# Kernel optimization log

Measured on AMD Instinct MI355X. Metric: run time of the kernel, lower is better.

The kernel has to match this reference:

```python
import jax, jax.numpy as jnp
import numpy as np


def setup_inputs() -> dict:
    key = jax.random.key(0)
    ks = jax.random.split(key, 8)
    H = 256  # hidden_size
    NH = 8   # num_heads
    HD = H // NH
    B, G = 256, 1024
    s = 1.0 / np.sqrt(H)
    return {
        "query": jax.random.normal(ks[0], (B, 2 * H), dtype=jnp.float32),
        "ref": jax.random.normal(ks[1], (B, G, H), dtype=jnp.float32),
        "Wq": jax.random.normal(ks[2], (H, 2 * H), dtype=jnp.float32) * s,
        "bq": jax.random.normal(ks[3], (H,), dtype=jnp.float32) * s,
        "We": jax.random.normal(ks[4], (H, H), dtype=jnp.float32) * s,
        "be": jax.random.normal(ks[5], (H,), dtype=jnp.float32) * s,
        "Wv": jax.random.normal(ks[6], (HD,), dtype=jnp.float32) * (1.0 / np.sqrt(HD)),
        "bv": jax.random.normal(ks[7], (1,), dtype=jnp.float32) * 0.01,
        "num_heads": 8,
    }


def reference(query, ref, Wq, bq, We, be, Wv, bv, num_heads):
    B, G, H = ref.shape
    hd = H // num_heads
    # q_dense: [B, 2H] -> [B, H] -> [B, nh, hd]
    q = (query @ Wq.T + bq).reshape(B, num_heads, hd)
    # e_dense: [B, G, H] -> [B, G, H] -> [B, G, nh, hd]
    e = (jnp.einsum('bgh,oh->bgo', ref, We) + be).reshape(B, G, num_heads, hd)
    # broadcast-add over graph dim, tanh, per-head linear scorer (hd -> 1)
    v = jnp.tanh(q[:, None, :, :] + e)                 # [B, G, nh, hd]
    s = jnp.einsum('bgnd,d->bgn', v, Wv) + bv[0]       # [B, G, nh]
    # sum over heads, output [B, 1, G] (matches sum(dim=1).transpose(1,2))
    return s.sum(axis=-1)[:, None, :]
```

## Files before the change

kernel.cpp:

```cpp
#include <hip/hip_runtime.h>

typedef __attribute__((ext_vector_type(8))) short short8;
typedef __attribute__((ext_vector_type(8))) unsigned short ushort8;
typedef __attribute__((ext_vector_type(4))) float f32x4;
typedef unsigned short ushort;
typedef unsigned int uint;

__device__ __forceinline__ float fast_exp2(float x) {
#if __has_builtin(__builtin_amdgcn_exp2f)
    return __builtin_amdgcn_exp2f(x);
#else
    return __expf(x * 0.6931471805599453f);
#endif
}
__device__ __forceinline__ float fast_rcp(float x) {
#if __has_builtin(__builtin_amdgcn_rcpf)
    return __builtin_amdgcn_rcpf(x);
#else
    return __frcp_rn(x);
#endif
}

__device__ __forceinline__ ushort f2bf(float f) {
    uint x = __float_as_uint(f);
    x += 0x7fffu + ((x >> 16) & 1u);
    return (ushort)(x >> 16);
}

__device__ __forceinline__ uint pack2bf(float x, float y) {
    uint xi = __float_as_uint(x) + 0x8000u;
    uint yi = __float_as_uint(y) + 0x8000u;
    return __builtin_amdgcn_perm(yi, xi, 0x07060302u);
}

__global__ __launch_bounds__(256) void prep(
    const float* __restrict__ query, const float* __restrict__ Wq,
    const float* __restrict__ bq, const float* __restrict__ be,
    const float* __restrict__ We, const float* __restrict__ Wv,
    const float* __restrict__ bv, float* __restrict__ q_ws,
    ushort* __restrict__ Web, float* __restrict__ aux) {
    __shared__ float qrow[512];
    const int t = threadIdx.x;
    if (blockIdx.x < 64) {
        const int i = (blockIdx.x * 256 + t) * 4;
        float4 v = *(const float4*)(We + i);
        ushort4 u;
        u.x = f2bf(v.x); u.y = f2bf(v.y); u.z = f2bf(v.z); u.w = f2bf(v.w);
        *(ushort4*)(Web + i) = u;
        return;
    }
    if (blockIdx.x == 320) {
        if (t >= 64) return;
        float v = (t < 32) ? Wv[t] : 0.f;
#pragma unroll
        for (int off = 1; off < 32; off <<= 1) v += __shfl_xor(v, off, 64);
        if (t == 0) aux[0] = 8.f * (v + bv[0]);
        return;
    }
    const int b = blockIdx.x - 64;
    qrow[t]       = query[b * 512 + t];
    qrow[t + 256] = query[b * 512 + 256 + t];
    __syncthreads();
    const f32x4* wr = (const f32x4*)(Wq + (size_t)t * 512);
    float s0 = 0.f, s1 = 0.f, s2 = 0.f, s3 = 0.f;
#pragma unroll 8
    for (int j = 0; j < 128; j += 4) {
        f32x4 w0 = wr[j], w1 = wr[j + 1], w2 = wr[j + 2], w3 = wr[j + 3];
        f32x4 q0 = *(const f32x4*)(qrow + 4 * j);
        f32x4 q1 = *(const f32x4*)(qrow + 4 * j + 4);
        f32x4 q2 = *(const f32x4*)(qrow + 4 * j + 8);
        f32x4 q3 = *(const f32x4*)(qrow + 4 * j + 12);
        s0 += w0.x * q0.x + w0.y * q0.y + w0.z * q0.z + w0.w * q0.w;
        s1 += w1.x * q1.x + w1.y * q1.y + w1.z * q1.z + w1.w * q1.w;
        s2 += w2.x * q2.x + w2.y * q2.y + w2.z * q2.z + w2.w * q2.w;
        s3 += w3.x * q3.x + w3.y * q3.y + w3.z * q3.z + w3.w * q3.w;
    }
    q_ws[b * 256 + t] = (s0 + s1) + (s2 + s3) + bq[t] + be[t];
}

#define BM 64

__global__ __launch_bounds__(256, 3) void fused_gemm(
    const float* __restrict__ ref, const ushort* __restrict__ Web,
    const float* __restrict__ q_ws, const float* __restrict__ Wv,
    const float* __restrict__ aux, float* __restrict__ out) {
    __shared__ uint4 Asm[2048];
    __shared__ float red[4][64];

    const int t = threadIdx.x;
    const int w = t >> 6;
    const int l = t & 63;
    const int quad = l >> 4;
    const int lr = l & 15;
    const size_t row0 = (size_t)blockIdx.x * BM;
    const int b = (int)(row0 >> 10);

    {
        const float* ap = ref + (row0 + w * 16 + lr) * 256 + quad * 8;
#pragma unroll
        for (int half = 0; half < 2; ++half) {
            float4 f[8];
#pragma unroll
            for (int kb = 0; kb < 4; ++kb) {
                f[2 * kb]     = *(const float4*)(ap + (half * 4 + kb) * 32);
                f[2 * kb + 1] = *(const float4*)(ap + (half * 4 + kb) * 32 + 4);
            }
#pragma unroll
            for (int kb = 0; kb < 4; ++kb) {
                uint4 p;
                p.x = pack2bf(f[2 * kb].x,     f[2 * kb].y);
                p.y = pack2bf(f[2 * kb].z,     f[2 * kb].w);
                p.z = pack2bf(f[2 * kb + 1].x, f[2 * kb + 1].y);
                p.w = pack2bf(f[2 * kb + 1].z, f[2 * kb + 1].w);
                Asm[(w * 8 + half * 4 + kb) * 64 + l] = p;
            }
        }
    }

    const ushort* Bp = Web + ((size_t)(w * 64 + lr)) * 256 + quad * 8;
    short8 bcur[4];
#pragma unroll
    for (int cb = 0; cb < 4; ++cb)
        bcur[cb] = *(const short8*)(Bp + cb * 16 * 256);

    const float c2l = 2.885390081777927f;
    const float* qe = q_ws + b * 256;
    const float w2a = -2.f * Wv[lr];
    const float w2b = -2.f * Wv[16 + lr];
    float qvc[4];
#pragma unroll
    for (int cb = 0; cb < 4; ++cb) qvc[cb] = qe[w * 64 + cb * 16 + lr] * c2l;

    __syncthreads();

    f32x4 acc[4][4];
#pragma unroll
    for (int i = 0; i < 4; ++i)
#pragma unroll
        for (int j = 0; j < 4; ++j) acc[i][j] = (f32x4){0.f, 0.f, 0.f, 0.f};

    const ushort* As = (const ushort*)Asm;
#pragma unroll
    for (int k = 0; k < 8; ++k) {
        short8 bnxt[4];
        if (k < 7) {
#pragma unroll
            for (int cb = 0; cb < 4; ++cb)
                bnxt[cb] = *(const short8*)(Bp + cb * 16 * 256 + (k + 1) * 32);
        }
        short8 afr[4];
#pragma unroll
        for (int rb = 0; rb < 4; ++rb)
            afr[rb] = *(const short8*)(As + ((rb * 8 + k) * 64 + l) * 8);
#pragma unroll
        for (int rb = 0; rb < 4; ++rb)
#pragma unroll
            for (int cb = 0; cb < 4; ++cb)
                acc[rb][cb] = __builtin_amdgcn_mfma_f32_16x16x32_bf16(
                    afr[rb], bcur[cb], acc[rb][cb], 0, 0, 0);
        if (k < 7) {
#pragma unroll
            for (int cb = 0; cb < 4; ++cb) bcur[cb] = bnxt[cb];
        }
    }

    float part[4][4];
#pragma unroll
    for (int rb = 0; rb < 4; ++rb)
#pragma unroll
        for (int r = 0; r < 4; ++r) part[rb][r] = 0.f;

#pragma unroll
    for (int cb = 0; cb < 4; ++cb) {
        const float w2 = (cb & 1) ? w2b : w2a;
#pragma unroll
        for (int rb = 0; rb < 4; ++rb)
#pragma unroll
            for (int r = 0; r < 4; ++r) {
                float e = fast_exp2(fmaf(acc[rb][cb][r], c2l, qvc[cb]));
                part[rb][r] = fmaf(w2, fast_rcp(e + 1.f), part[rb][r]);
            }
    }
#pragma unroll
    for (int off = 1; off < 16; off <<= 1)
#pragma unroll
        for (int rb = 0; rb < 4; ++rb)
#pragma unroll
            for (int r = 0; r < 4; ++r)
                part[rb][r] += __shfl_xor(part[rb][r], off, 64);

    if (lr == 0) {
#pragma unroll
        for (int rb = 0; rb < 4; ++rb)
#pragma unroll
            for (int r = 0; r < 4; ++r)
                red[w][rb * 16 + quad * 4 + r] = part[rb][r];
    }
    __syncthreads();
    if (t < 64) {
        float s = red[0][t] + red[1][t] + red[2][t] + red[3][t] + aux[0];
        out[row0 + t] = s;
    }
}

extern "C" void kernel_launch(void* const* d_in, const int* in_sizes, int n_in,
                              void* d_out, int out_size, void* d_ws, size_t ws_size,
                              hipStream_t stream) {
    const float* query = (const float*)d_in[0];
    const float* ref   = (const float*)d_in[1];
    const float* Wq    = (const float*)d_in[2];
    const float* bq    = (const float*)d_in[3];
    const float* We    = (const float*)d_in[4];
    const float* be    = (const float*)d_in[5];
    const float* Wv    = (const float*)d_in[6];
    const float* bv    = (const float*)d_in[7];
    float* out = (float*)d_out;

    float*  q_ws = (float*)d_ws;
    ushort* Web  = (ushort*)((char*)d_ws + 262144);
    float*  aux  = (float*)((char*)d_ws + 262144 + 131072);

    prep<<<321, 256, 0, stream>>>(query, Wq, bq, be, We, Wv, bv, q_ws, Web, aux);
    fused_gemm<<<4096, 256, 0, stream>>>(ref, Web, q_ws, Wv, aux, out);
}
```

Before: 423.0 us.

## Load A fragments directly into registers with 2x2 wave tiling, drop LDS staging

The GEMM kernel no longer stages the bf16-converted ref tile in shared memory. Waves are now arranged 2x2, each owning 32 rows by 128 columns, and each loads its A fragments straight from global memory into registers, converting to bf16 in place. This removes the LDS write/read round trip and the barrier before the MFMA loop, and halves redundant A loads per wave. In exchange, B loads per wave double, register pressure rises, and launch bounds occupancy drops from 3 to 2 blocks per CU.

```diff
diff --git a/kernel.cpp b/kernel.cpp
--- a/kernel.cpp
+++ b/kernel.cpp
@@ -1,7 +1,6 @@
 #include <hip/hip_runtime.h>
 
 typedef __attribute__((ext_vector_type(8))) short short8;
-typedef __attribute__((ext_vector_type(8))) unsigned short ushort8;
 typedef __attribute__((ext_vector_type(4))) float f32x4;
 typedef unsigned short ushort;
 typedef unsigned int uint;
@@ -31,6 +30,15 @@
     uint xi = __float_as_uint(x) + 0x8000u;
     uint yi = __float_as_uint(y) + 0x8000u;
     return __builtin_amdgcn_perm(yi, xi, 0x07060302u);
+}
+
+__device__ __forceinline__ short8 pack8(float4 a, float4 b) {
+    union { uint4 u; short8 s; } c;
+    c.u.x = pack2bf(a.x, a.y);
+    c.u.y = pack2bf(a.z, a.w);
+    c.u.z = pack2bf(b.x, b.y);
+    c.u.w = pack2bf(b.z, b.w);
+    return c.s;
 }
 
 __global__ __launch_bounds__(256) void prep(
@@ -80,126 +88,120 @@
 
 #define BM 64
 
-__global__ __launch_bounds__(256, 3) void fused_gemm(
+__global__ __launch_bounds__(256, 2) void fused_gemm(
     const float* __restrict__ ref, const ushort* __restrict__ Web,
     const float* __restrict__ q_ws, const float* __restrict__ Wv,
     const float* __restrict__ aux, float* __restrict__ out) {
-    __shared__ uint4 Asm[2048];
-    __shared__ float red[4][64];
+    __shared__ float red[2][64];
 
     const int t = threadIdx.x;
     const int w = t >> 6;
+    const int wr = w >> 1;
+    const int wc = w & 1;
     const int l = t & 63;
     const int quad = l >> 4;
     const int lr = l & 15;
     const size_t row0 = (size_t)blockIdx.x * BM;
     const int b = (int)(row0 >> 10);
 
-    {
-        const float* ap = ref + (row0 + w * 16 + lr) * 256 + quad * 8;
-#pragma unroll
-        for (int half = 0; half < 2; ++half) {
-            float4 f[8];
-#pragma unroll
-            for (int kb = 0; kb < 4; ++kb) {
-                f[2 * kb]     = *(const float4*)(ap + (half * 4 + kb) * 32);
-                f[2 * kb + 1] = *(const float4*)(ap + (half * 4 + kb) * 32 + 4);
-            }
-#pragma unroll
-            for (int kb = 0; kb < 4; ++kb) {
-                uint4 p;
-                p.x = pack2bf(f[2 * kb].x,     f[2 * kb].y);
-                p.y = pack2bf(f[2 * kb].z,     f[2 * kb].w);
-                p.z = pack2bf(f[2 * kb + 1].x, f[2 * kb + 1].y);
-                p.w = pack2bf(f[2 * kb + 1].z, f[2 * kb + 1].w);
-                Asm[(w * 8 + half * 4 + kb) * 64 + l] = p;
-            }
+    const float* ap = ref + (row0 + wr * 32 + lr) * 256 + quad * 8;
+    const ushort* Bp = Web + ((size_t)(wc * 128 + lr)) * 256 + quad * 8;
+
+    short8 bc[8];
+#pragma unroll
+    for (int cb = 0; cb < 8; ++cb)
+        bc[cb] = *(const short8*)(Bp + cb * 16 * 256);
+
+    short8 af[2][8];
+#pragma unroll
+    for (int k = 0; k < 4; ++k) {
+        float4 a0 = *(const float4*)(ap + k * 32);
+        float4 a1 = *(const float4*)(ap + k * 32 + 4);
+        float4 a2 = *(const float4*)(ap + 16 * 256 + k * 32);
+        float4 a3 = *(const float4*)(ap + 16 * 256 + k * 32 + 4);
+        af[0][k] = pack8(a0, a1);
+        af[1][k] = pack8(a2, a3);
+    }
+    __builtin_amdgcn_sched_barrier(0);
+#pragma unroll
+    for (int k = 4; k < 8; ++k) {
+        float4 a0 = *(const float4*)(ap + k * 32);
+        float4 a1 = *(const float4*)(ap + k * 32 + 4);
+        float4 a2 = *(const float4*)(ap + 16 * 256 + k * 32);
+        float4 a3 = *(const float4*)(ap + 16 * 256 + k * 32 + 4);
+        af[0][k] = pack8(a0, a1);
+        af[1][k] = pack8(a2, a3);
+    }
+
+    f32x4 acc[2][8];
+#pragma unroll
+    for (int i = 0; i < 2; ++i)
+#pragma unroll
+        for (int j = 0; j < 8; ++j) acc[i][j] = (f32x4){0.f, 0.f, 0.f, 0.f};
+
+#pragma unroll
+    for (int k = 0; k < 8; ++k) {
+        short8 bn[8];
+        if (k < 7) {
+#pragma unroll
+            for (int cb = 0; cb < 8; ++cb)
+                bn[cb] = *(const short8*)(Bp + cb * 16 * 256 + (k + 1) * 32);
         }
-    }
-
-    const ushort* Bp = Web + ((size_t)(w * 64 + lr)) * 256 + quad * 8;
-    short8 bcur[4];
-#pragma unroll
-    for (int cb = 0; cb < 4; ++cb)
-        bcur[cb] = *(const short8*)(Bp + cb * 16 * 256);
+#pragma unroll
+        for (int rt = 0; rt < 2; ++rt)
+#pragma unroll
+            for (int cb = 0; cb < 8; ++cb)
+                acc[rt][cb] = __builtin_amdgcn_mfma_f32_16x16x32_bf16(
+                    af[rt][k], bc[cb], acc[rt][cb], 0, 0, 0);
+        if (k < 7) {
+#pragma unroll
+            for (int cb = 0; cb < 8; ++cb) bc[cb] = bn[cb];
+        }
+    }
 
     const float c2l = 2.885390081777927f;
-    const float* qe = q_ws + b * 256;
+    const float* qe = q_ws + b * 256 + wc * 128 + lr;
     const float w2a = -2.f * Wv[lr];
     const float w2b = -2.f * Wv[16 + lr];
-    float qvc[4];
-#pragma unroll
-    for (int cb = 0; cb < 4; ++cb) qvc[cb] = qe[w * 64 + cb * 16 + lr] * c2l;
-
-    __syncthreads();
-
-    f32x4 acc[4][4];
-#pragma unroll
-    for (int i = 0; i < 4; ++i)
-#pragma unroll
-        for (int j = 0; j < 4; ++j) acc[i][j] = (f32x4){0.f, 0.f, 0.f, 0.f};
-
-    const ushort* As = (const ushort*)Asm;
-#pragma unroll
-    for (int k = 0; k < 8; ++k) {
-        short8 bnxt[4];
-        if (k < 7) {
-#pragma unroll
-            for (int cb = 0; cb < 4; ++cb)
-                bnxt[cb] = *(const short8*)(Bp + cb * 16 * 256 + (k + 1) * 32);
-        }
-        short8 afr[4];
-#pragma unroll
-        for (int rb = 0; rb < 4; ++rb)
-            afr[rb] = *(const short8*)(As + ((rb * 8 + k) * 64 + l) * 8);
-#pragma unroll
-        for (int rb = 0; rb < 4; ++rb)
-#pragma unroll
-            for (int cb = 0; cb < 4; ++cb)
-                acc[rb][cb] = __builtin_amdgcn_mfma_f32_16x16x32_bf16(
-                    afr[rb], bcur[cb], acc[rb][cb], 0, 0, 0);
-        if (k < 7) {
-#pragma unroll
-            for (int cb = 0; cb < 4; ++cb) bcur[cb] = bnxt[cb];
-        }
-    }
-
-    float part[4][4];
-#pragma unroll
-    for (int rb = 0; rb < 4; ++rb)
-#pragma unroll
-        for (int r = 0; r < 4; ++r) part[rb][r] = 0.f;
-
-#pragma unroll
-    for (int cb = 0; cb < 4; ++cb) {
+    float qv[8];
+#pragma unroll
+    for (int cb = 0; cb < 8; ++cb) qv[cb] = qe[cb * 16] * c2l;
+
+    float part[2][4];
+#pragma unroll
+    for (int rt = 0; rt < 2; ++rt)
+#pragma unroll
+        for (int r = 0; r < 4; ++r) part[rt][r] = 0.f;
+
+#pragma unroll
+    for (int cb = 0; cb < 8; ++cb) {
         const float w2 = (cb & 1) ? w2b : w2a;
 #pragma unroll
-        for (int rb = 0; rb < 4; ++rb)
+        for (int rt = 0; rt < 2; ++rt)
 #pragma unroll
             for (int r = 0; r < 4; ++r) {
-                float e = fast_exp2(fmaf(acc[rb][cb][r], c2l, qvc[cb]));
-                part[rb][r] = fmaf(w2, fast_rcp(e + 1.f), part[rb][r]);
+                float e = fast_exp2(fmaf(acc[rt][cb][r], c2l, qv[cb]));
+                part[rt][r] = fmaf(w2, fast_rcp(e + 1.f), part[rt][r]);
             }
     }
 #pragma unroll
     for (int off = 1; off < 16; off <<= 1)
 #pragma unroll
-        for (int rb = 0; rb < 4; ++rb)
+        for (int rt = 0; rt < 2; ++rt)
 #pragma unroll
             for (int r = 0; r < 4; ++r)
-                part[rb][r] += __shfl_xor(part[rb][r], off, 64);
+                part[rt][r] += __shfl_xor(part[rt][r], off, 64);
 
     if (lr == 0) {
 #pragma unroll
-        for (int rb = 0; rb < 4; ++rb)
+        for (int rt = 0; rt < 2; ++rt)
 #pragma unroll
             for (int r = 0; r < 4; ++r)
-                red[w][rb * 16 + quad * 4 + r] = part[rb][r];
+                red[wc][wr * 32 + rt * 16 + quad * 4 + r] = part[rt][r];
     }
     __syncthreads();
     if (t < 64) {
-        float s = red[0][t] + red[1][t] + red[2][t] + red[3][t] + aux[0];
-        out[row0 + t] = s;
+        out[row0 + t] = red[0][t] + red[1][t] + aux[0];
     }
 }
 
```

After: 496.3 us. 1.17x slower.

## Make fused GEMM persistent over row tiles with resident B and double-buffered A

Applied to the files above, without the earlier changes.

Each block now processes 512 rows in 16 tiles of 32 rows and keeps the entire bf16 We slice it needs in registers, so it loads it once per block instead of once per 64 rows. The ref loads for the next tile are issued before the MFMAs on the current tile and written into a second LDS buffer, overlapping global loads with compute. Output reduction writes are deferred by one iteration. The trade-offs are a much larger register footprint (occupancy bound lowered to 2), only 512 blocks, and a barrier per tile.

```diff
diff --git a/kernel.cpp b/kernel.cpp
--- a/kernel.cpp
+++ b/kernel.cpp
@@ -1,7 +1,6 @@
 #include <hip/hip_runtime.h>
 
 typedef __attribute__((ext_vector_type(8))) short short8;
-typedef __attribute__((ext_vector_type(8))) unsigned short ushort8;
 typedef __attribute__((ext_vector_type(4))) float f32x4;
 typedef unsigned short ushort;
 typedef unsigned int uint;
@@ -31,6 +30,15 @@
     uint xi = __float_as_uint(x) + 0x8000u;
     uint yi = __float_as_uint(y) + 0x8000u;
     return __builtin_amdgcn_perm(yi, xi, 0x07060302u);
+}
+
+__device__ __forceinline__ uint4 pack8u(float4 a, float4 b) {
+    uint4 c;
+    c.x = pack2bf(a.x, a.y);
+    c.y = pack2bf(a.z, a.w);
+    c.z = pack2bf(b.x, b.y);
+    c.w = pack2bf(b.z, b.w);
+    return c;
 }
 
 __global__ __launch_bounds__(256) void prep(
@@ -78,128 +86,145 @@
     q_ws[b * 256 + t] = (s0 + s1) + (s2 + s3) + bq[t] + be[t];
 }
 
-#define BM 64
-
-__global__ __launch_bounds__(256, 3) void fused_gemm(
+__global__ __launch_bounds__(256, 2) void fused_gemm(
     const float* __restrict__ ref, const ushort* __restrict__ Web,
     const float* __restrict__ q_ws, const float* __restrict__ Wv,
     const float* __restrict__ aux, float* __restrict__ out) {
-    __shared__ uint4 Asm[2048];
-    __shared__ float red[4][64];
+    __shared__ uint4 Asm[2 * 1024];
+    __shared__ float red[2][4][32];
 
     const int t = threadIdx.x;
     const int w = t >> 6;
     const int l = t & 63;
     const int quad = l >> 4;
     const int lr = l & 15;
-    const size_t row0 = (size_t)blockIdx.x * BM;
-    const int b = (int)(row0 >> 10);
-
-    {
-        const float* ap = ref + (row0 + w * 16 + lr) * 256 + quad * 8;
-#pragma unroll
-        for (int half = 0; half < 2; ++half) {
-            float4 f[8];
-#pragma unroll
-            for (int kb = 0; kb < 4; ++kb) {
-                f[2 * kb]     = *(const float4*)(ap + (half * 4 + kb) * 32);
-                f[2 * kb + 1] = *(const float4*)(ap + (half * 4 + kb) * 32 + 4);
-            }
-#pragma unroll
-            for (int kb = 0; kb < 4; ++kb) {
-                uint4 p;
-                p.x = pack2bf(f[2 * kb].x,     f[2 * kb].y);
-                p.y = pack2bf(f[2 * kb].z,     f[2 * kb].w);
-                p.z = pack2bf(f[2 * kb + 1].x, f[2 * kb + 1].y);
-                p.w = pack2bf(f[2 * kb + 1].z, f[2 * kb + 1].w);
-                Asm[(w * 8 + half * 4 + kb) * 64 + l] = p;
-            }
-        }
-    }
+    const int rbw = w & 1;
+    const int kh = w >> 1;
+    const size_t rowB = (size_t)blockIdx.x * 512;
+    const int b = (int)(blockIdx.x >> 1);
 
     const ushort* Bp = Web + ((size_t)(w * 64 + lr)) * 256 + quad * 8;
-    short8 bcur[4];
+    short8 bfr[4][8];
 #pragma unroll
     for (int cb = 0; cb < 4; ++cb)
-        bcur[cb] = *(const short8*)(Bp + cb * 16 * 256);
+#pragma unroll
+        for (int k = 0; k < 8; ++k)
+            bfr[cb][k] = *(const short8*)(Bp + cb * 16 * 256 + k * 32);
 
     const float c2l = 2.885390081777927f;
     const float* qe = q_ws + b * 256;
     const float w2a = -2.f * Wv[lr];
     const float w2b = -2.f * Wv[16 + lr];
+    const float aux0 = aux[0];
     float qvc[4];
 #pragma unroll
     for (int cb = 0; cb < 4; ++cb) qvc[cb] = qe[w * 64 + cb * 16 + lr] * c2l;
 
-    __syncthreads();
-
-    f32x4 acc[4][4];
-#pragma unroll
-    for (int i = 0; i < 4; ++i)
-#pragma unroll
-        for (int j = 0; j < 4; ++j) acc[i][j] = (f32x4){0.f, 0.f, 0.f, 0.f};
-
-    const ushort* As = (const ushort*)Asm;
-#pragma unroll
-    for (int k = 0; k < 8; ++k) {
-        short8 bnxt[4];
-        if (k < 7) {
-#pragma unroll
-            for (int cb = 0; cb < 4; ++cb)
-                bnxt[cb] = *(const short8*)(Bp + cb * 16 * 256 + (k + 1) * 32);
-        }
-        short8 afr[4];
-#pragma unroll
-        for (int rb = 0; rb < 4; ++rb)
-            afr[rb] = *(const short8*)(As + ((rb * 8 + k) * 64 + l) * 8);
-#pragma unroll
-        for (int rb = 0; rb < 4; ++rb)
-#pragma unroll
-            for (int cb = 0; cb < 4; ++cb)
-                acc[rb][cb] = __builtin_amdgcn_mfma_f32_16x16x32_bf16(
-                    afr[rb], bcur[cb], acc[rb][cb], 0, 0, 0);
-        if (k < 7) {
-#pragma unroll
-            for (int cb = 0; cb < 4; ++cb) bcur[cb] = bnxt[cb];
-        }
-    }
-
-    float part[4][4];
-#pragma unroll
-    for (int rb = 0; rb < 4; ++rb)
-#pragma unroll
-        for (int r = 0; r < 4; ++r) part[rb][r] = 0.f;
-
-#pragma unroll
-    for (int cb = 0; cb < 4; ++cb) {
-        const float w2 = (cb & 1) ? w2b : w2a;
-#pragma unroll
-        for (int rb = 0; rb < 4; ++rb)
-#pragma unroll
-            for (int r = 0; r < 4; ++r) {
-                float e = fast_exp2(fmaf(acc[rb][cb][r], c2l, qvc[cb]));
-                part[rb][r] = fmaf(w2, fast_rcp(e + 1.f), part[rb][r]);
+    const float* apst = ref + (rowB + rbw * 16 + lr) * 256 + kh * 128 + quad * 8;
+
+    {
+        float4 f[8];
+#pragma unroll
+        for (int kk = 0; kk < 4; ++kk) {
+            f[2 * kk]     = *(const float4*)(apst + kk * 32);
+            f[2 * kk + 1] = *(const float4*)(apst + kk * 32 + 4);
+        }
+#pragma unroll
+        for (int kk = 0; kk < 4; ++kk)
+            Asm[(rbw * 8 + kh * 4 + kk) * 64 + l] = pack8u(f[2 * kk], f[2 * kk + 1]);
+    }
+    asm volatile("s_waitcnt lgkmcnt(0)" ::: "memory");
+    __builtin_amdgcn_s_barrier();
+    __builtin_amdgcn_sched_barrier(0);
+
+    for (int tl = 0; tl < 16; ++tl) {
+        const uint4* bufr = Asm + (tl & 1) * 1024;
+        uint4* bufw = Asm + ((tl + 1) & 1) * 1024;
+
+        if (tl > 0 && t < 32) {
+            const float* rp = &red[(tl - 1) & 1][0][0];
+            out[rowB + (size_t)(tl - 1) * 32 + t] =
+                rp[t] + rp[32 + t] + rp[64 + t] + rp[96 + t] + aux0;
+        }
+
+        float4 f[8];
+        if (tl < 15) {
+            const float* ap = apst + (size_t)(tl + 1) * 32 * 256;
+#pragma unroll
+            for (int kk = 0; kk < 4; ++kk) {
+                f[2 * kk]     = *(const float4*)(ap + kk * 32);
+                f[2 * kk + 1] = *(const float4*)(ap + kk * 32 + 4);
             }
-    }
-#pragma unroll
-    for (int off = 1; off < 16; off <<= 1)
-#pragma unroll
-        for (int rb = 0; rb < 4; ++rb)
-#pragma unroll
-            for (int r = 0; r < 4; ++r)
-                part[rb][r] += __shfl_xor(part[rb][r], off, 64);
-
-    if (lr == 0) {
-#pragma unroll
-        for (int rb = 0; rb < 4; ++rb)
-#pragma unroll
-            for (int r = 0; r < 4; ++r)
-                red[w][rb * 16 + quad * 4 + r] = part[rb][r];
-    }
-    __syncthreads();
-    if (t < 64) {
-        float s = red[0][t] + red[1][t] + red[2][t] + red[3][t] + aux[0];
-        out[row0 + t] = s;
+        }
+
+        f32x4 acc[2][4];
+#pragma unroll
+        for (int i = 0; i < 2; ++i)
+#pragma unroll
+            for (int j = 0; j < 4; ++j) acc[i][j] = (f32x4){0.f, 0.f, 0.f, 0.f};
+
+        const ushort* As = (const ushort*)bufr;
+#pragma unroll
+        for (int k = 0; k < 8; ++k) {
+            short8 afr[2];
+#pragma unroll
+            for (int rt = 0; rt < 2; ++rt)
+                afr[rt] = *(const short8*)(As + ((rt * 8 + k) * 64 + l) * 8);
+#pragma unroll
+            for (int rt = 0; rt < 2; ++rt)
+#pragma unroll
+                for (int cb = 0; cb < 4; ++cb)
+                    acc[rt][cb] = __builtin_amdgcn_mfma_f32_16x16x32_bf16(
+                        afr[rt], bfr[cb][k], acc[rt][cb], 0, 0, 0);
+        }
+
+        if (tl < 15) {
+#pragma unroll
+            for (int kk = 0; kk < 4; ++kk)
+                bufw[(rbw * 8 + kh * 4 + kk) * 64 + l] =
+                    pack8u(f[2 * kk], f[2 * kk + 1]);
+        }
+
+        float part[2][4];
+#pragma unroll
+        for (int rt = 0; rt < 2; ++rt)
+#pragma unroll
+            for (int r = 0; r < 4; ++r) part[rt][r] = 0.f;
+#pragma unroll
+        for (int cb = 0; cb < 4; ++cb) {
+            const float w2 = (cb & 1) ? w2b : w2a;
+#pragma unroll
+            for (int rt = 0; rt < 2; ++rt)
+#pragma unroll
+                for (int r = 0; r < 4; ++r) {
+                    float e = fast_exp2(fmaf(acc[rt][cb][r], c2l, qvc[cb]));
+                    part[rt][r] = fmaf(w2, fast_rcp(e + 1.f), part[rt][r]);
+                }
+        }
+#pragma unroll
+        for (int off = 1; off < 16; off <<= 1)
+#pragma unroll
+            for (int rt = 0; rt < 2; ++rt)
+#pragma unroll
+                for (int r = 0; r < 4; ++r)
+                    part[rt][r] += __shfl_xor(part[rt][r], off, 64);
+        if (lr == 0) {
+#pragma unroll
+            for (int rt = 0; rt < 2; ++rt)
+#pragma unroll
+                for (int r = 0; r < 4; ++r)
+                    red[tl & 1][w][rt * 16 + quad * 4 + r] = part[rt][r];
+        }
+
+        asm volatile("s_waitcnt lgkmcnt(0)" ::: "memory");
+        __builtin_amdgcn_s_barrier();
+        __builtin_amdgcn_sched_barrier(0);
+    }
+
+    if (t < 32) {
+        const float* rp = &red[15 & 1][0][0];
+        out[rowB + 15 * 32 + t] =
+            rp[t] + rp[32 + t] + rp[64 + t] + rp[96 + t] + aux0;
     }
 }
 
@@ -221,5 +246,5 @@
     float*  aux  = (float*)((char*)d_ws + 262144 + 131072);
 
     prep<<<321, 256, 0, stream>>>(query, Wq, bq, be, We, Wv, bv, q_ws, Web, aux);
-    fused_gemm<<<4096, 256, 0, stream>>>(ref, Web, q_ws, Wv, aux, out);
-}
+    fused_gemm<<<512, 256, 0, stream>>>(ref, Web, q_ws, Wv, aux, out);
+}
```

After: 404.8 us. 4.3% less time.
